# Performance work log

Measured on AMD Instinct MI355X. Metric: run time of the kernel, lower is better.

The kernel has to match this reference:

```python
import jax, jax.numpy as jnp
import numpy as np

B = 32        # num graphs
N = 512       # nodes per graph (equal-sized blocks)
HID = 512     # hidden_dim
H = 8         # num_heads
E = 262144    # num edges
ED = 16       # edge feature dim


def setup_inputs() -> dict:
    key = jax.random.key(0)
    ks = jax.random.split(key, 12)
    x = jax.random.normal(ks[0], (B * N, HID), jnp.float32)
    # contiguous, sorted graph assignment (equal-sized graphs)
    batch = jnp.repeat(jnp.arange(B, dtype=jnp.int64), N)
    # within-graph random edges
    g = jax.random.randint(ks[1], (E,), 0, B)
    src = g * N + jax.random.randint(ks[2], (E,), 0, N)
    dst = g * N + jax.random.randint(ks[3], (E,), 0, N)
    edge_index = jnp.stack([src, dst]).astype(jnp.int64)
    edge_attr = jax.random.normal(ks[4], (E, ED), jnp.float32)
    s = 1.0 / np.sqrt(HID).astype(np.float32)
    Wq = jax.random.normal(ks[5], (HID, HID), jnp.float32) * s
    Wk = jax.random.normal(ks[6], (HID, HID), jnp.float32) * s
    Wv = jax.random.normal(ks[7], (HID, HID), jnp.float32) * s
    Wo = jax.random.normal(ks[8], (HID, HID), jnp.float32) * s
    We = jax.random.normal(ks[9], (ED, H), jnp.float32) * (1.0 / np.sqrt(ED).astype(np.float32))
    bq = jnp.zeros((HID,), jnp.float32)
    bk = jnp.zeros((HID,), jnp.float32)
    bv = jnp.zeros((HID,), jnp.float32)
    bo = jnp.zeros((HID,), jnp.float32)
    be = jnp.zeros((H,), jnp.float32)
    return dict(x=x, batch=batch, edge_index=edge_index, edge_attr=edge_attr,
                Wq=Wq, bq=bq, Wk=Wk, bk=bk, Wv=Wv, bv=bv, Wo=Wo, bo=bo,
                We=We, be=be, num_graphs=B)


def reference(x, batch, edge_index, edge_attr, Wq, bq, Wk, bk, Wv, bv, Wo, bo, We, be, num_graphs):
    n_total, hid = x.shape
    n = n_total // num_graphs           # nodes per graph (equal blocks)
    hd = hid // H                       # head_dim
    scale = 1.0 / jnp.sqrt(jnp.asarray(hd, x.dtype))
    q = (x @ Wq + bq).reshape(num_graphs, n, H, hd)
    k = (x @ Wk + bk).reshape(num_graphs, n, H, hd)
    v = (x @ Wv + bv).reshape(num_graphs, n, H, hd)
    # per-graph dense scores: [B, n(query), m(key), H]
    attn = jnp.einsum('bnhd,bmhd->bnmh', q, k) * scale
    # edge-bias scatter-add (edges are intra-graph; local coords via div/mod)
    eb = edge_attr @ We + be                      # [E, H]
    b_idx = edge_index[0] // n
    loc_src = edge_index[0] % n
    loc_dst = edge_index[1] % n
    attn = attn.at[b_idx, loc_src, loc_dst].add(eb)
    # softmax over key axis (torch dim=1 of 'nmh' == axis 2 here)
    attn = jax.nn.softmax(attn, axis=2)
    out = jnp.einsum('bnmh,bmhd->bnhd', attn, v).reshape(n_total, hid)
    return out @ Wo + bo
```

## Files before the change

### kernel.cpp

```cpp
#include <hip/hip_runtime.h>
#include <stdint.h>

typedef unsigned short u16;
typedef __bf16 bf16x8 __attribute__((ext_vector_type(8)));
typedef short  short8 __attribute__((ext_vector_type(8)));
typedef float  f32x4  __attribute__((ext_vector_type(4)));
typedef float  float4v __attribute__((ext_vector_type(4)));
typedef uint32_t u32x2 __attribute__((ext_vector_type(2)));

#define NG    32
#define NPG   512
#define HIDD  512
#define NH    8
#define HD    64
#define NE    262144
#define NNODE (NG*NPG)

__device__ __forceinline__ float fexp2(float x) { return __builtin_amdgcn_exp2f(x); }

__device__ __forceinline__ u16 f2bf(float f) {
  union { float f; uint32_t u; } x; x.f = f;
  uint32_t r = x.u + 0x7FFFu + ((x.u >> 16) & 1u);
  return (u16)(r >> 16);
}
__device__ __forceinline__ float bf2f(u16 b) {
  union { uint32_t u; float f; } x; x.u = ((uint32_t)b) << 16;
  return x.f;
}
__device__ __forceinline__ bf16x8 ldfrag(const u16* p) {
  short8 t = *(const short8*)p;
  return __builtin_bit_cast(bf16x8, t);
}
__device__ __forceinline__ f32x4 mfma16(bf16x8 a, bf16x8 b, f32x4 c) {
  return __builtin_amdgcn_mfma_f32_16x16x32_bf16(a, b, c, 0, 0, 0);
}
__device__ __forceinline__ void gl2lds16(const void* g, void* l) {
  __builtin_amdgcn_global_load_lds((const __attribute__((address_space(1))) void*)g,
                                   (__attribute__((address_space(3))) void*)l, 16, 0, 0);
}
__device__ __forceinline__ void st(u16* p, float v)   { *p = f2bf(v); }
__device__ __forceinline__ void st(float* p, float v) { *p = v; }


__global__ void k_cast_x(const float* __restrict__ x, u16* __restrict__ xb) {
  size_t i = ((size_t)blockIdx.x * 256 + threadIdx.x) * 8;
  float4v v0 = *(const float4v*)(x + i);
  float4v v1 = *(const float4v*)(x + i + 4);
  short8 r;
  r[0]=(short)f2bf(v0[0]); r[1]=(short)f2bf(v0[1]); r[2]=(short)f2bf(v0[2]); r[3]=(short)f2bf(v0[3]);
  r[4]=(short)f2bf(v1[0]); r[5]=(short)f2bf(v1[1]); r[6]=(short)f2bf(v1[2]); r[7]=(short)f2bf(v1[3]);
  *(short8*)(xb + i) = r;
}

__global__ void k_transw(const float* __restrict__ W0, const float* __restrict__ W1,
                         const float* __restrict__ W2, const float* __restrict__ W3,
                         u16* __restrict__ wt) {
  const float* W = blockIdx.z==0 ? W0 : blockIdx.z==1 ? W1 : blockIdx.z==2 ? W2 : W3;
  u16* out = wt + (size_t)blockIdx.z * HIDD * HIDD;
  __shared__ float tl[32][33];
  int tx = threadIdx.x, ty = threadIdx.y;
  int x0 = blockIdx.x * 32, y0 = blockIdx.y * 32;
  #pragma unroll
  for (int i = 0; i < 4; ++i) tl[ty + i*8][tx] = W[(size_t)(y0 + ty + i*8) * HIDD + x0 + tx];
  __syncthreads();
  #pragma unroll
  for (int i = 0; i < 4; ++i) out[(size_t)(x0 + ty + i*8) * HIDD + (y0 + tx)] = f2bf(tl[tx][ty + i*8]);
}

__global__ void k_count2(const int* __restrict__ ei, int* __restrict__ counts) {
  int e = blockIdx.x * 256 + threadIdx.x;
  int src = ei[e];
  int dl  = ei[NE + e] & (NPG - 1);
  atomicAdd(&counts[src * 8 + (dl >> 6)], 1);
}

__global__ void k_scan_a(const int* __restrict__ counts, int* __restrict__ rowstart,
                         int* __restrict__ bsum) {
  __shared__ int arr[256];
  int t = threadIdx.x;
  int i = blockIdx.x * 256 + t;
  int c = counts[i];
  arr[t] = c;
  __syncthreads();
  for (int off = 1; off < 256; off <<= 1) {
    int v = (t >= off) ? arr[t - off] : 0;
    __syncthreads();
    arr[t] += v;
    __syncthreads();
  }
  rowstart[i] = arr[t] - c;
  if (t == 255) bsum[blockIdx.x] = arr[255];
}
__global__ void k_scan_b(int* __restrict__ bsum) {
  __shared__ int arr[512];
  int t = threadIdx.x;
  int c = bsum[t];
  arr[t] = c;
  __syncthreads();
  for (int off = 1; off < 512; off <<= 1) {
    int v = (t >= off) ? arr[t - off] : 0;
    __syncthreads();
    arr[t] += v;
    __syncthreads();
  }
  bsum[t] = arr[t] - c;
}
__global__ void k_scan_c(const int* __restrict__ bsum, int* __restrict__ rowstart) {
  int i = blockIdx.x * 256 + threadIdx.x;
  rowstart[i] += bsum[blockIdx.x];
  if (i == 0) rowstart[131072] = NE;
}

__global__ void k_fill(const int* __restrict__ ei, const float* __restrict__ ea,
                       const float* __restrict__ We, const float* __restrict__ be,
                       const int* __restrict__ rowstart, int* __restrict__ cursor,
                       uint32_t* __restrict__ packed) {
  __shared__ float w[128];
  __shared__ float bb[8];
  int t = threadIdx.x;
  if (t < 128) w[t] = We[t];
  if (t < 8)   bb[t] = be[t];
  __syncthreads();
  int e = blockIdx.x * 256 + t;
  int src = ei[e];
  int dl  = ei[NE + e] & (NPG - 1);
  const float* ap = ea + (size_t)e * 16;
  float a[16];
  #pragma unroll
  for (int i = 0; i < 16; i += 4) {
    float4v v = *(const float4v*)(ap + i);
    a[i]=v[0]; a[i+1]=v[1]; a[i+2]=v[2]; a[i+3]=v[3];
  }
  float acc[8];
  #pragma unroll
  for (int hh = 0; hh < 8; ++hh) acc[hh] = bb[hh];
  #pragma unroll
  for (int d = 0; d < 16; ++d)
    #pragma unroll
    for (int hh = 0; hh < 8; ++hh) acc[hh] += a[d] * w[d*8 + hh];
  int bin = src * 8 + (dl >> 6);
  int pos = atomicAdd(&cursor[bin], 1);
  size_t base = ((size_t)(rowstart[bin] + pos)) * 8;
  #pragma unroll
  for (int hh = 0; hh < 8; ++hh) {
    float m = fexp2(acc[hh] * 1.44269504089f);
    union { _Float16 hf; u16 us; } cv; cv.hf = (_Float16)m;
    packed[base + hh] = (uint32_t)(dl & 63) | ((uint32_t)cv.us << 16);
  }
}


template <typename OT, bool VOUT>
__device__ void gemm_body(u16* smem, const u16* __restrict__ A, const u16* __restrict__ Bt,
                          const float* __restrict__ bias, OT* __restrict__ C,
                          u16* __restrict__ vtg) {
  const int tid = threadIdx.x;
  const int w = tid >> 6, l = tid & 63, lr = l & 15, lg = l >> 4;
  const int bm0 = blockIdx.y * 128, bn0 = blockIdx.x * 128;
  const int wr = w >> 1, wc = w & 1;
  f32x4 acc[4][4];
  #pragma unroll
  for (int i = 0; i < 4; ++i)
    #pragma unroll
    for (int j = 0; j < 4; ++j) acc[i][j] = (f32x4){0.f, 0.f, 0.f, 0.f};

  const int o1 = w * 1024 + l * 16;
  auto stageAB = [&](int kt, int buf) {
    #pragma unroll
    for (int rnd = 0; rnd < 2; ++rnd) {
      const int o = rnd * 4096 + o1;
      const int row = o >> 6, colb = o & 63;
      gl2lds16((const char*)A  + ((size_t)(bm0 + row) * HIDD + kt * 32) * 2 + colb,
               (char*)smem + buf * 8192 + o);
      gl2lds16((const char*)Bt + ((size_t)(bn0 + row) * HIDD + kt * 32) * 2 + colb,
               (char*)smem + 16384 + buf * 8192 + o);
    }
  };

  stageAB(0, 0);
  for (int kt = 0; kt < 16; ++kt) {
    if (kt < 15) {
      stageAB(kt + 1, (kt + 1) & 1);
      asm volatile("s_waitcnt vmcnt(4)" ::: "memory");
    } else {
      asm volatile("s_waitcnt vmcnt(0)" ::: "memory");
    }
    __syncthreads();
    const u16* Ab = smem + (kt & 1) * 4096;
    const u16* Bb = smem + 8192 + (kt & 1) * 4096;
    bf16x8 af[4], bfr[4];
    #pragma unroll
    for (int i = 0; i < 4; ++i) af[i]  = ldfrag(&Ab[(wr*64 + i*16 + lr) * 32 + lg*8]);
    #pragma unroll
    for (int j = 0; j < 4; ++j) bfr[j] = ldfrag(&Bb[(wc*64 + j*16 + lr) * 32 + lg*8]);
    #pragma unroll
    for (int i = 0; i < 4; ++i)
      #pragma unroll
      for (int j = 0; j < 4; ++j)
        acc[i][j] = mfma16(af[i], bfr[j], acc[i][j]);
    __syncthreads();
  }

  if constexpr (VOUT) {
    #pragma unroll
    for (int j = 0; j < 4; ++j) {
      const int d = j * 16 + lr;
      const float bv = bias[bn0 + wc*64 + j*16 + lr];
      #pragma unroll
      for (int i = 0; i < 4; ++i) {
        const int t4 = wc * 2 + wr;
        const int byteo = t4 * 8192 + d * 128 + ((i*32 + lg*8) ^ ((d & 7) << 4));
        uint32_t lo = (uint32_t)f2bf(acc[i][j][0] + bv) | ((uint32_t)f2bf(acc[i][j][1] + bv) << 16);
        uint32_t hi = (uint32_t)f2bf(acc[i][j][2] + bv) | ((uint32_t)f2bf(acc[i][j][3] + bv) << 16);
        *(u32x2*)((char*)smem + byteo) = (u32x2){lo, hi};
      }
    }
    __syncthreads();
    const int b = bm0 >> 9, kt0 = (bm0 & 511) >> 6, h0 = bn0 >> 6;
    #pragma unroll
    for (int t4 = 0; t4 < 4; ++t4) {
      size_t base = ((size_t)(b * 8 + h0 + (t4 >> 1)) * 8 + kt0 + (t4 & 1)) * 4096;
      #pragma unroll
      for (int rnd = 0; rnd < 2; ++rnd) {
        int idx = rnd * 256 + tid;
        *(short8*)(vtg + base + idx * 8) = *(const short8*)&smem[t4 * 4096 + idx * 8];
      }
    }
  } else {
    #pragma unroll
    for (int j = 0; j < 4; ++j) {
      const int col = bn0 + wc*64 + j*16 + lr;
      const float bv = bias[col];
      #pragma unroll
      for (int i = 0; i < 4; ++i) {
        const int row0 = bm0 + wr*64 + i*16 + lg*4;
        #pragma unroll
        for (int q = 0; q < 4; ++q)
          st(&C[(size_t)(row0 + q) * HIDD + col], acc[i][j][q] + bv);
      }
    }
  }
}

__global__ __launch_bounds__(256, 3) void k_gemm_qkv(
    const u16* __restrict__ A, const u16* __restrict__ Wt,
    const float* __restrict__ b0, const float* __restrict__ b1, const float* __restrict__ b2,
    u16* __restrict__ O0, u16* __restrict__ O1, u16* __restrict__ vtg) {
  __shared__ u16 smem[16384];
  int z = blockIdx.z;
  const u16* Bt = Wt + (size_t)z * HIDD * HIDD;
  if (z == 0)      gemm_body<u16, false>(smem, A, Bt, b0, O0, nullptr);
  else if (z == 1) gemm_body<u16, false>(smem, A, Bt, b1, O1, nullptr);
  else             gemm_body<u16, true >(smem, A, Bt, b2, nullptr, vtg);
}

__global__ __launch_bounds__(256, 3) void k_gemm_out(
    const u16* __restrict__ A, const u16* __restrict__ Bt,
    const float* __restrict__ bias, float* __restrict__ C) {
  __shared__ u16 smem[16384];
  gemm_body<float, false>(smem, A, Bt, bias, C, nullptr);
}


__global__ __launch_bounds__(256, 4) void k_attn(
    const u16* __restrict__ qb, const u16* __restrict__ kb, const u16* __restrict__ vtg,
    const uint32_t* __restrict__ packed, const int* __restrict__ rowstart2,
    u16* __restrict__ ab) {
  __shared__ u16 kl[2][4096];
  __shared__ u16 vl[2][4096];
  __shared__ u16 pl[4][1024];
  const int tid = threadIdx.x, w = tid >> 6, l = tid & 63, lr = l & 15, lg = l >> 4;

  const int id = blockIdx.x;
  const int nid = (id & 7) * 256 + (id >> 3);
  const int q0 = (nid & 7) * 64;
  const int h  = (nid >> 3) & 7;
  const int b  = nid >> 6;
  const int bh = b * 8 + h;
  const int row = w * 16 + lr;
  const int grow = b * NPG + q0 + row;
  u16* plw = &pl[w][0];
  const int pswz = (lr & 7) << 4;

  bf16x8 qf[2];
  {
    const u16* qp = qb + (size_t)grow * HIDD + h * HD + lg * 8;
    qf[0] = ldfrag(qp);
    qf[1] = ldfrag(qp + 32);
  }

  auto stageK = [&](int kt, int buf) {
    #pragma unroll
    for (int rnd = 0; rnd < 2; ++rnd) {
      int o = rnd * 4096 + w * 1024 + l * 16;
      int key = o >> 7, db = o & 127;
      int col = db ^ ((key & 7) << 4);
      gl2lds16((const char*)kb + ((size_t)(b * NPG + kt * 64 + key) * HIDD + h * HD) * 2 + col,
               (char*)kl + buf * 8192 + o);
    }
  };
  auto stageV = [&](int kt, int buf) {
    #pragma unroll
    for (int rnd = 0; rnd < 2; ++rnd) {
      int o = rnd * 4096 + w * 1024 + l * 16;
      gl2lds16((const char*)vtg + ((size_t)(bh * 8 + kt)) * 8192 + o,
               (char*)vl + buf * 8192 + o);
    }
  };

  const float c1 = 0.125f * 1.44269504089f;
  float m2 = -1e30f;
  float rowsum = 0.f;
  f32x4 oacc[4];
  #pragma unroll
  for (int dt = 0; dt < 4; ++dt) oacc[dt] = (f32x4){0.f, 0.f, 0.f, 0.f};

  stageK(0, 0); stageV(0, 0); stageK(1, 1); stageV(1, 1);

  for (int kt = 0; kt < 8; ++kt) {
    if (kt < 7) asm volatile("s_waitcnt vmcnt(4)" ::: "memory");
    else        asm volatile("s_waitcnt vmcnt(0)" ::: "memory");
    __syncthreads();

    const u16* kB = kl[kt & 1];
    f32x4 s4[4];
    #pragma unroll
    for (int sub = 0; sub < 4; ++sub) {
      s4[sub] = (f32x4){0.f, 0.f, 0.f, 0.f};
      int key = sub * 16 + lr;
      #pragma unroll
      for (int ks = 0; ks < 2; ++ks) {
        int db = ((ks * 32 + lg * 8) * 2) ^ ((key & 7) << 4);
        bf16x8 kf = ldfrag(&kB[(key * 128 + db) >> 1]);
        s4[sub] = mfma16(kf, qf[ks], s4[sub]);
      }
    }

    float tm = s4[0][0];
    #pragma unroll
    for (int sub = 0; sub < 4; ++sub)
      #pragma unroll
      for (int e = 0; e < 4; ++e) tm = fmaxf(tm, s4[sub][e]);
    tm = fmaxf(tm, __shfl_xor(tm, 16, 64));
    tm = fmaxf(tm, __shfl_xor(tm, 32, 64));
    float m2n = fmaxf(m2, tm * c1);
    float rsc = fexp2(m2 - m2n);
    m2 = m2n;
    rowsum *= rsc;
    #pragma unroll
    for (int dt = 0; dt < 4; ++dt) oacc[dt] *= rsc;

    #pragma unroll
    for (int sub = 0; sub < 4; ++sub) {
      float p0 = fexp2(__builtin_fmaf(s4[sub][0], c1, -m2n));
      float p1 = fexp2(__builtin_fmaf(s4[sub][1], c1, -m2n));
      float p2 = fexp2(__builtin_fmaf(s4[sub][2], c1, -m2n));
      float p3 = fexp2(__builtin_fmaf(s4[sub][3], c1, -m2n));
      rowsum += (p0 + p1) + (p2 + p3);
      uint32_t lo = (uint32_t)f2bf(p0) | ((uint32_t)f2bf(p1) << 16);
      uint32_t hi = (uint32_t)f2bf(p2) | ((uint32_t)f2bf(p3) << 16);
      *(u32x2*)((char*)plw + lr * 128 + ((sub * 32 + lg * 8) ^ pswz)) = (u32x2){lo, hi};
    }
    asm volatile("s_waitcnt lgkmcnt(0)" ::: "memory");
    __builtin_amdgcn_sched_barrier(0);

    {
      int e0 = rowstart2[grow * 8 + kt];
      int e1 = rowstart2[grow * 8 + kt + 1];
      float delta = 0.f;
      for (int s = e0; s < e1; ++s) {
        uint32_t u = packed[(size_t)s * 8 + h];
        int dl = (int)(u & 63u);
        if ((dl & 3) == lg) {
          union { u16 us; _Float16 hf; } cv; cv.us = (u16)(u >> 16);
          float mult = (float)cv.hf;
          int idx = (lr * 128 + ((dl * 2) ^ pswz)) >> 1;
          float old = bf2f(plw[idx]);
          u16 nb = f2bf(old * mult);
          plw[idx] = nb;
          delta += bf2f(nb) - old;
        }
      }
      rowsum += delta;
    }
    asm volatile("s_waitcnt lgkmcnt(0)" ::: "memory");
    __builtin_amdgcn_sched_barrier(0);

    const u16* vB = vl[kt & 1];
    #pragma unroll
    for (int ks = 0; ks < 2; ++ks) {
      bf16x8 pa = ldfrag(&plw[(lr * 128 + ((ks * 64 + lg * 16) ^ pswz)) >> 1]);
      #pragma unroll
      for (int dt = 0; dt < 4; ++dt) {
        int d = dt * 16 + lr;
        bf16x8 vf = ldfrag(&vB[(d * 128 + ((ks * 64 + lg * 16) ^ ((d & 7) << 4))) >> 1]);
        oacc[dt] = mfma16(vf, pa, oacc[dt]);
      }
    }

    __syncthreads();
    if (kt < 6) { stageK(kt + 2, kt & 1); stageV(kt + 2, kt & 1); }
  }

  float tot = rowsum + __shfl_xor(rowsum, 16, 64);
  tot += __shfl_xor(tot, 32, 64);
  float inv = 1.0f / tot;
  #pragma unroll
  for (int dt = 0; dt < 4; ++dt) {
    uint32_t lo = (uint32_t)f2bf(oacc[dt][0] * inv) | ((uint32_t)f2bf(oacc[dt][1] * inv) << 16);
    uint32_t hi = (uint32_t)f2bf(oacc[dt][2] * inv) | ((uint32_t)f2bf(oacc[dt][3] * inv) << 16);
    *(u32x2*)(ab + (size_t)grow * HIDD + h * HD + dt * 16 + lg * 4) = (u32x2){lo, hi};
  }
}


extern "C" void kernel_launch(void* const* d_in, const int* in_sizes, int n_in,
                              void* d_out, int out_size, void* d_ws, size_t ws_size,
                              hipStream_t stream) {
  const float* x  = (const float*)d_in[0];
  const int*   ei = (const int*)d_in[2];
  const float* ea = (const float*)d_in[3];
  const float* Wq = (const float*)d_in[4];  const float* bq = (const float*)d_in[5];
  const float* Wk = (const float*)d_in[6];  const float* bk = (const float*)d_in[7];
  const float* Wv = (const float*)d_in[8];  const float* bv = (const float*)d_in[9];
  const float* Wo = (const float*)d_in[10]; const float* bo = (const float*)d_in[11];
  const float* We = (const float*)d_in[12]; const float* be = (const float*)d_in[13];

  char* ws = (char*)d_ws;
  const size_t MB = 1 << 20;
  u16*  xb  = (u16*)(ws);
  u16*  wt  = (u16*)(ws + 16*MB);
  u16*  qbp = (u16*)(ws + 18*MB);
  u16*  kbp = (u16*)(ws + 34*MB);
  u16*  vtg = (u16*)(ws + 50*MB);
  uint32_t* packed = (uint32_t*)(ws + 66*MB);
  int*  rowstart2 = (int*)(ws + 74*MB);
  int*  bsum      = (int*)(ws + 74*MB + 640*1024);
  int*  counts2  = (int*)(ws + 50*MB);
  int*  cursor2  = (int*)(ws + 50*MB + 512*1024);
  u16*  ab = xb;

  (void)hipMemsetAsync(counts2, 0, 2 * 512 * 1024, stream);

  k_cast_x<<<dim3(NNODE * HIDD / (256 * 8)), 256, 0, stream>>>(x, xb);
  k_transw<<<dim3(16, 16, 4), dim3(32, 8, 1), 0, stream>>>(Wq, Wk, Wv, Wo, wt);
  k_count2<<<dim3(NE / 256), 256, 0, stream>>>(ei, counts2);
  k_scan_a<<<dim3(512), 256, 0, stream>>>(counts2, rowstart2, bsum);
  k_scan_b<<<dim3(1), 512, 0, stream>>>(bsum);
  k_scan_c<<<dim3(512), 256, 0, stream>>>(bsum, rowstart2);
  k_fill<<<dim3(NE / 256), 256, 0, stream>>>(ei, ea, We, be, rowstart2, cursor2, packed);

  k_gemm_qkv<<<dim3(HIDD / 128, NNODE / 128, 3), 256, 0, stream>>>(
      xb, wt, bq, bk, bv, qbp, kbp, vtg);

  k_attn<<<dim3(2048), 256, 0, stream>>>(qbp, kbp, vtg, packed, rowstart2, ab);

  k_gemm_out<<<dim3(HIDD / 128, NNODE / 128, 1), 256, 0, stream>>>(
      ab, wt + (size_t)3 * HIDD * HIDD, bo, (float*)d_out);
}
```

Baseline: 181.3 us.

## Lazy softmax rescale, prefetch edge row offsets, setprio around MFMA, hardware bf16 pack

The attention kernel now rescales the running max and accumulators only when some lane's new tile max exceeds the current max by more than a threshold, which skips the exp and multiply work on most tiles. The per-tile edge-range offsets are loaded one iteration ahead to hide global load latency. Wave priority is raised around the MFMA blocks. Manual float-to-bf16 rounding is replaced by the compiler's native conversion so it can use packed convert instructions. The lazy rescale lets exponentials reach up to about 2^8 before renormalisation, which relies on fp32 headroom and slightly changes the numerics.

```diff
diff --git a/kernel.cpp b/kernel.cpp
--- a/kernel.cpp
+++ b/kernel.cpp
@@ -26,6 +26,10 @@
 __device__ __forceinline__ float bf2f(u16 b) {
   union { uint32_t u; float f; } x; x.u = ((uint32_t)b) << 16;
   return x.f;
+}
+__device__ __forceinline__ uint32_t pkbf(float a, float b) {
+  __bf16 x = (__bf16)a, y = (__bf16)b;
+  return (uint32_t)__builtin_bit_cast(u16, x) | ((uint32_t)__builtin_bit_cast(u16, y) << 16);
 }
 __device__ __forceinline__ bf16x8 ldfrag(const u16* p) {
   short8 t = *(const short8*)p;
@@ -210,8 +214,8 @@
       for (int i = 0; i < 4; ++i) {
         const int t4 = wc * 2 + wr;
         const int byteo = t4 * 8192 + d * 128 + ((i*32 + lg*8) ^ ((d & 7) << 4));
-        uint32_t lo = (uint32_t)f2bf(acc[i][j][0] + bv) | ((uint32_t)f2bf(acc[i][j][1] + bv) << 16);
-        uint32_t hi = (uint32_t)f2bf(acc[i][j][2] + bv) | ((uint32_t)f2bf(acc[i][j][3] + bv) << 16);
+        uint32_t lo = pkbf(acc[i][j][0] + bv, acc[i][j][1] + bv);
+        uint32_t hi = pkbf(acc[i][j][2] + bv, acc[i][j][3] + bv);
         *(u32x2*)((char*)smem + byteo) = (u32x2){lo, hi};
       }
     }
@@ -317,13 +321,18 @@
 
   stageK(0, 0); stageV(0, 0); stageK(1, 1); stageV(1, 1);
 
+  int eA = rowstart2[grow * 8];
+  int eB = rowstart2[grow * 8 + 1];
+
   for (int kt = 0; kt < 8; ++kt) {
+    int eC = (kt < 7) ? rowstart2[grow * 8 + kt + 2] : 0;
     if (kt < 7) asm volatile("s_waitcnt vmcnt(4)" ::: "memory");
     else        asm volatile("s_waitcnt vmcnt(0)" ::: "memory");
     __syncthreads();
 
     const u16* kB = kl[kt & 1];
     f32x4 s4[4];
+    __builtin_amdgcn_s_setprio(1);
     #pragma unroll
     for (int sub = 0; sub < 4; ++sub) {
       s4[sub] = (f32x4){0.f, 0.f, 0.f, 0.f};
@@ -335,6 +344,7 @@
         s4[sub] = mfma16(kf, qf[ks], s4[sub]);
       }
     }
+    __builtin_amdgcn_s_setprio(0);
 
     float tm = s4[0][0];
     #pragma unroll
@@ -343,32 +353,33 @@
       for (int e = 0; e < 4; ++e) tm = fmaxf(tm, s4[sub][e]);
     tm = fmaxf(tm, __shfl_xor(tm, 16, 64));
     tm = fmaxf(tm, __shfl_xor(tm, 32, 64));
-    float m2n = fmaxf(m2, tm * c1);
-    float rsc = fexp2(m2 - m2n);
-    m2 = m2n;
-    rowsum *= rsc;
-    #pragma unroll
-    for (int dt = 0; dt < 4; ++dt) oacc[dt] *= rsc;
+    float tmc = tm * c1;
+    if (__any(tmc > m2 + 8.0f)) {
+      float m2n = fmaxf(m2, tmc);
+      float rsc = fexp2(m2 - m2n);
+      m2 = m2n;
+      rowsum *= rsc;
+      #pragma unroll
+      for (int dt = 0; dt < 4; ++dt) oacc[dt] *= rsc;
+    }
 
     #pragma unroll
     for (int sub = 0; sub < 4; ++sub) {
-      float p0 = fexp2(__builtin_fmaf(s4[sub][0], c1, -m2n));
-      float p1 = fexp2(__builtin_fmaf(s4[sub][1], c1, -m2n));
-      float p2 = fexp2(__builtin_fmaf(s4[sub][2], c1, -m2n));
-      float p3 = fexp2(__builtin_fmaf(s4[sub][3], c1, -m2n));
+      float p0 = fexp2(__builtin_fmaf(s4[sub][0], c1, -m2));
+      float p1 = fexp2(__builtin_fmaf(s4[sub][1], c1, -m2));
+      float p2 = fexp2(__builtin_fmaf(s4[sub][2], c1, -m2));
+      float p3 = fexp2(__builtin_fmaf(s4[sub][3], c1, -m2));
       rowsum += (p0 + p1) + (p2 + p3);
-      uint32_t lo = (uint32_t)f2bf(p0) | ((uint32_t)f2bf(p1) << 16);
-      uint32_t hi = (uint32_t)f2bf(p2) | ((uint32_t)f2bf(p3) << 16);
+      uint32_t lo = pkbf(p0, p1);
+      uint32_t hi = pkbf(p2, p3);
       *(u32x2*)((char*)plw + lr * 128 + ((sub * 32 + lg * 8) ^ pswz)) = (u32x2){lo, hi};
     }
     asm volatile("s_waitcnt lgkmcnt(0)" ::: "memory");
     __builtin_amdgcn_sched_barrier(0);
 
     {
-      int e0 = rowstart2[grow * 8 + kt];
-      int e1 = rowstart2[grow * 8 + kt + 1];
       float delta = 0.f;
-      for (int s = e0; s < e1; ++s) {
+      for (int s = eA; s < eB; ++s) {
         uint32_t u = packed[(size_t)s * 8 + h];
         int dl = (int)(u & 63u);
         if ((dl & 3) == lg) {
@@ -387,6 +398,7 @@
     __builtin_amdgcn_sched_barrier(0);
 
     const u16* vB = vl[kt & 1];
+    __builtin_amdgcn_s_setprio(1);
     #pragma unroll
     for (int ks = 0; ks < 2; ++ks) {
       bf16x8 pa = ldfrag(&plw[(lr * 128 + ((ks * 64 + lg * 16) ^ pswz)) >> 1]);
@@ -397,9 +409,11 @@
         oacc[dt] = mfma16(vf, pa, oacc[dt]);
       }
     }
+    __builtin_amdgcn_s_setprio(0);
 
     __syncthreads();
     if (kt < 6) { stageK(kt + 2, kt & 1); stageV(kt + 2, kt & 1); }
+    eA = eB; eB = eC;
   }
 
   float tot = rowsum + __shfl_xor(rowsum, 16, 64);
@@ -407,8 +421,8 @@
   float inv = 1.0f / tot;
   #pragma unroll
   for (int dt = 0; dt < 4; ++dt) {
-    uint32_t lo = (uint32_t)f2bf(oacc[dt][0] * inv) | ((uint32_t)f2bf(oacc[dt][1] * inv) << 16);
-    uint32_t hi = (uint32_t)f2bf(oacc[dt][2] * inv) | ((uint32_t)f2bf(oacc[dt][3] * inv) << 16);
+    uint32_t lo = pkbf(oacc[dt][0] * inv, oacc[dt][1] * inv);
+    uint32_t hi = pkbf(oacc[dt][2] * inv, oacc[dt][3] * inv);
     *(u32x2*)(ab + (size_t)grow * HIDD + h * HD + dt * 16 + lg * 4) = (u32x2){lo, hi};
   }
 }
```

New measurement: 177.8 us. About the same (-2.0%).
